# Performance work log

Measured on AMD Instinct MI355X. Metric: run time of the kernel, lower is better.

## Reference

```python
import jax, jax.numpy as jnp
import numpy as np

K = 32
TEMPERATURE = 0.1
RTOL, ATOL = 1e-5, 1e-5


def _embed(x, W1, b1, W2, b2, W3, b3):
    h = jax.nn.gelu(x @ W1.T + b1, approximate=False)
    h = jax.nn.gelu(h @ W2.T + b2, approximate=False)
    return jax.nn.sigmoid(h @ W3.T + b3)


def setup_inputs() -> dict:
    key = jax.random.key(0)
    ks = jax.random.split(key, 9)
    Q, N, D_IN, D_E = 256, 16384, 256, 64
    s = lambda fan_in: 1.0 / np.sqrt(fan_in)
    return {
        "x": jax.random.normal(ks[0], (Q, D_IN), jnp.float32),
        "support_x": jax.random.normal(ks[1], (N, D_IN), jnp.float32),
        "support_labels": jax.random.uniform(ks[2], (N, 1), jnp.float32),
        "W1": jax.random.normal(ks[3], (D_E, D_IN), jnp.float32) * s(D_IN),
        "b1": jax.random.normal(ks[4], (D_E,), jnp.float32) * s(D_IN),
        "W2": jax.random.normal(ks[5], (D_E, D_E), jnp.float32) * s(D_E),
        "b2": jax.random.normal(ks[6], (D_E,), jnp.float32) * s(D_E),
        "W3": jax.random.normal(ks[7], (D_E, D_E), jnp.float32) * s(D_E),
        "b3": jax.random.normal(ks[8], (D_E,), jnp.float32) * s(D_E),
    }


def reference(x, support_x, support_labels, W1, b1, W2, b2, W3, b3):
    # query embeddings [Q, D]; support embeddings [N, D] (set_support is no_grad)
    q = _embed(x, W1, b1, W2, b2, W3, b3)
    s = jax.lax.stop_gradient(_embed(support_x, W1, b1, W2, b2, W3, b3))
    # torch.cdist p=2 via expanded squared distances
    d2 = (jnp.sum(q * q, -1)[:, None] + jnp.sum(s * s, -1)[None, :]
          - 2.0 * (q @ s.T))
    dist = jnp.sqrt(jnp.maximum(d2, 0.0))  # [Q, N]
    # isclose mask: |q - s| <= atol + rtol*|s|, all over feature dim
    close = jnp.abs(q[:, None, :] - s[None, :, :]) <= (ATOL + RTOL * jnp.abs(s)[None, :, :])
    mask = jnp.all(close, axis=-1)  # [Q, N]
    dist = jnp.where(mask, jnp.inf, dist)
    # top-k smallest distances
    neg_top, idx = jax.lax.top_k(-dist, K)  # [Q, K]
    topd = -neg_top
    neighbor_labels = support_labels[idx].squeeze(-1)  # [Q, K]
    weights = jax.nn.softmax(-topd / TEMPERATURE, axis=1)
    return jnp.sum(weights * neighbor_labels, axis=1)  # [Q]
```

## Files before the change

### kernel.cpp

```cpp
#include <hip/hip_runtime.h>
#include <math.h>

#define D_IN   256
#define D_E    64
#define N_SUP  16384
#define NQ     256
#define KSEL   32
#define RTOLC  1e-5f
#define ATOLC  1e-5f
#define INV_T  10.0f

#define CHUNK  512
#define NCH    32
#define QG     16
#define NQG    16

typedef unsigned long long ull;

__device__ __forceinline__ float gelu_exact(float x) {
    return 0.5f * x * (1.0f + erff(x * 0.70710678118654752440f));
}

__global__ __launch_bounds__(128) void embed_kernel(
    const float* __restrict__ sx, const float* __restrict__ x,
    const float* __restrict__ W1, const float* __restrict__ b1,
    const float* __restrict__ W2, const float* __restrict__ b2,
    const float* __restrict__ W3, const float* __restrict__ b3,
    float* __restrict__ s_emb, float* __restrict__ s_norm,
    float* __restrict__ q_emb, float* __restrict__ q_norm)
{
    __shared__ float xc[2][64][36];
    __shared__ float wc[2][64][68];
    __shared__ float nsq[32][17];

    const int tid = threadIdx.x;
    const int rg  = tid >> 4;
    const int fg  = tid & 15;
    const bool isq = blockIdx.x >= (N_SUP / 32);
    const int rowbase = isq ? (int)(blockIdx.x - N_SUP / 32) * 32
                            : (int)blockIdx.x * 32;
    const float* src = (isq ? x : sx) + (size_t)rowbase * D_IN;

    #define STAGE_X(kc_, b_)                                                   \
        {                                                                      \
            _Pragma("unroll")                                                  \
            for (int i_ = 0; i_ < 4; ++i_) {                                   \
                int g_ = i_ * 128 + tid;                                       \
                int row_ = g_ >> 4, c4_ = g_ & 15;                             \
                float4 v_ = *reinterpret_cast<const float4*>(                  \
                    src + (size_t)row_ * D_IN + (kc_) * 64 + c4_ * 4);         \
                xc[b_][c4_ * 4 + 0][row_] = v_.x;                              \
                xc[b_][c4_ * 4 + 1][row_] = v_.y;                              \
                xc[b_][c4_ * 4 + 2][row_] = v_.z;                              \
                xc[b_][c4_ * 4 + 3][row_] = v_.w;                              \
            }                                                                  \
        }
    #define STAGE_W1(kc_, b_)                                                  \
        {                                                                      \
            _Pragma("unroll")                                                  \
            for (int i_ = 0; i_ < 8; ++i_) {                                   \
                int g_ = i_ * 128 + tid;                                       \
                int f_ = g_ >> 4, c4_ = g_ & 15;                               \
                float4 w_ = *reinterpret_cast<const float4*>(                  \
                    W1 + (size_t)f_ * D_IN + (kc_) * 64 + c4_ * 4);            \
                wc[b_][c4_ * 4 + 0][f_] = w_.x;                                \
                wc[b_][c4_ * 4 + 1][f_] = w_.y;                                \
                wc[b_][c4_ * 4 + 2][f_] = w_.z;                                \
                wc[b_][c4_ * 4 + 3][f_] = w_.w;                                \
            }                                                                  \
        }
    #define STAGE_WSQ(Wp_, b_)                                                 \
        {                                                                      \
            _Pragma("unroll")                                                  \
            for (int i_ = 0; i_ < 8; ++i_) {                                   \
                int g_ = i_ * 128 + tid;                                       \
                int f_ = g_ >> 4, c4_ = g_ & 15;                               \
                float4 w_ = *reinterpret_cast<const float4*>(                  \
                    (Wp_) + (size_t)f_ * D_E + c4_ * 4);                       \
                wc[b_][c4_ * 4 + 0][f_] = w_.x;                                \
                wc[b_][c4_ * 4 + 1][f_] = w_.y;                                \
                wc[b_][c4_ * 4 + 2][f_] = w_.z;                                \
                wc[b_][c4_ * 4 + 3][f_] = w_.w;                                \
            }                                                                  \
        }
    #define GEMM64(XB_, WB_, ACC_)                                             \
        {                                                                      \
            _Pragma("unroll 8")                                                \
            for (int k_ = 0; k_ < 64; ++k_) {                                  \
                float4 xv_ = *reinterpret_cast<const float4*>(&XB_[k_][rg * 4]); \
                float4 wv_ = *reinterpret_cast<const float4*>(&WB_[k_][fg * 4]); \
                ACC_[0][0] = fmaf(wv_.x, xv_.x, ACC_[0][0]);                   \
                ACC_[0][1] = fmaf(wv_.y, xv_.x, ACC_[0][1]);                   \
                ACC_[0][2] = fmaf(wv_.z, xv_.x, ACC_[0][2]);                   \
                ACC_[0][3] = fmaf(wv_.w, xv_.x, ACC_[0][3]);                   \
                ACC_[1][0] = fmaf(wv_.x, xv_.y, ACC_[1][0]);                   \
                ACC_[1][1] = fmaf(wv_.y, xv_.y, ACC_[1][1]);                   \
                ACC_[1][2] = fmaf(wv_.z, xv_.y, ACC_[1][2]);                   \
                ACC_[1][3] = fmaf(wv_.w, xv_.y, ACC_[1][3]);                   \
                ACC_[2][0] = fmaf(wv_.x, xv_.z, ACC_[2][0]);                   \
                ACC_[2][1] = fmaf(wv_.y, xv_.z, ACC_[2][1]);                   \
                ACC_[2][2] = fmaf(wv_.z, xv_.z, ACC_[2][2]);                   \
                ACC_[2][3] = fmaf(wv_.w, xv_.z, ACC_[2][3]);                   \
                ACC_[3][0] = fmaf(wv_.x, xv_.w, ACC_[3][0]);                   \
                ACC_[3][1] = fmaf(wv_.y, xv_.w, ACC_[3][1]);                   \
                ACC_[3][2] = fmaf(wv_.z, xv_.w, ACC_[3][2]);                   \
                ACC_[3][3] = fmaf(wv_.w, xv_.w, ACC_[3][3]);                   \
            }                                                                  \
        }

    float4 bv1 = *reinterpret_cast<const float4*>(b1 + fg * 4);
    float acc[4][4];
    #pragma unroll
    for (int j = 0; j < 4; ++j) {
        acc[j][0] = bv1.x; acc[j][1] = bv1.y; acc[j][2] = bv1.z; acc[j][3] = bv1.w;
    }
    STAGE_X(0, 0); STAGE_W1(0, 0);
    __syncthreads();
    #pragma unroll
    for (int kc = 0; kc < 4; ++kc) {
        const int b = kc & 1;
        if (kc < 3) { STAGE_X(kc + 1, b ^ 1); STAGE_W1(kc + 1, b ^ 1); }
        GEMM64(xc[b], wc[b], acc);
        __syncthreads();
    }

    #pragma unroll
    for (int j = 0; j < 4; ++j)
        #pragma unroll
        for (int i = 0; i < 4; ++i)
            xc[0][fg * 4 + i][rg * 4 + j] = gelu_exact(acc[j][i]);
    STAGE_WSQ(W2, 0);
    STAGE_WSQ(W3, 1);
    __syncthreads();

    float4 bv2 = *reinterpret_cast<const float4*>(b2 + fg * 4);
    float a2[4][4];
    #pragma unroll
    for (int j = 0; j < 4; ++j) {
        a2[j][0] = bv2.x; a2[j][1] = bv2.y; a2[j][2] = bv2.z; a2[j][3] = bv2.w;
    }
    GEMM64(xc[0], wc[0], a2);
    #pragma unroll
    for (int j = 0; j < 4; ++j)
        #pragma unroll
        for (int i = 0; i < 4; ++i)
            xc[1][fg * 4 + i][rg * 4 + j] = gelu_exact(a2[j][i]);
    __syncthreads();

    float4 bv3 = *reinterpret_cast<const float4*>(b3 + fg * 4);
    float a3[4][4];
    #pragma unroll
    for (int j = 0; j < 4; ++j) {
        a3[j][0] = bv3.x; a3[j][1] = bv3.y; a3[j][2] = bv3.z; a3[j][3] = bv3.w;
    }
    GEMM64(xc[1], wc[1], a3);

    float* E   = isq ? q_emb  : s_emb;
    float* Nrm = isq ? q_norm : s_norm;
    #pragma unroll
    for (int j = 0; j < 4; ++j) {
        float e0 = 1.0f / (1.0f + expf(-a3[j][0]));
        float e1 = 1.0f / (1.0f + expf(-a3[j][1]));
        float e2 = 1.0f / (1.0f + expf(-a3[j][2]));
        float e3 = 1.0f / (1.0f + expf(-a3[j][3]));
        *reinterpret_cast<float4*>(E + (size_t)(rowbase + rg * 4 + j) * D_E + fg * 4)
            = make_float4(e0, e1, e2, e3);
        a3[j][0] = fmaf(e0, e0, fmaf(e1, e1, fmaf(e2, e2, e3 * e3)));
    }
    #pragma unroll
    for (int j = 0; j < 4; ++j) nsq[rg * 4 + j][fg] = a3[j][0];
    __syncthreads();
    if (tid < 32) {
        float s = 0.0f;
        #pragma unroll
        for (int g = 0; g < 16; ++g) s += nsq[tid][g];
        Nrm[rowbase + tid] = s;
    }
    #undef STAGE_X
    #undef STAGE_W1
    #undef STAGE_WSQ
    #undef GEMM64
}

__global__ __launch_bounds__(512, 1) void knn_phaseA(
    const float* __restrict__ s_emb, const float* __restrict__ s_norm,
    const float* __restrict__ q_emb, const float* __restrict__ q_norm,
    const float* __restrict__ labels, ull* __restrict__ cand)
{
    __shared__ float tile[2][64 * 68];
    __shared__ ull   win_l[QG][KSEL];

    const int tid  = threadIdx.x;
    const int lane = tid & 63;
    const int wid  = tid >> 6;
    const int qg   = blockIdx.x >> 5;
    const int sc   = blockIdx.x & 31;
    const int qiu  = __builtin_amdgcn_readfirstlane(qg * QG + 2 * wid);
    const float* q0 = q_emb + (size_t)qiu * D_E;
    const float* q1 = q0 + D_E;
    const float  qn0 = q_norm[qiu];
    const float  qn1 = q_norm[qiu + 1];

    #pragma unroll
    for (int i = 0; i < 2; ++i) {
        int g = i * 512 + tid;
        int row = g >> 4, c4 = g & 15;
        float4 v = *reinterpret_cast<const float4*>(
            s_emb + (size_t)(sc * CHUNK + row) * D_E + c4 * 4);
        *reinterpret_cast<float4*>(&tile[0][row * 68 + c4 * 4]) = v;
    }
    __syncthreads();

    float d2a[8], d2b[8];
    #pragma unroll
    for (int s = 0; s < 8; ++s) {
        const int b = s & 1;
        float4 p0, p1;
        if (s < 7) {
            p0 = *reinterpret_cast<const float4*>(
                s_emb + (size_t)(sc * CHUNK + (s + 1) * 64 + (tid >> 4)) * D_E + (tid & 15) * 4);
            p1 = *reinterpret_cast<const float4*>(
                s_emb + (size_t)(sc * CHUNK + (s + 1) * 64 + ((512 + tid) >> 4)) * D_E + (tid & 15) * 4);
        }
        const float* tr = &tile[b][lane * 68];
        float a0 = 0.0f, a1 = 0.0f;
        #pragma unroll
        for (int c = 0; c < 16; ++c) {
            float4 sv = *reinterpret_cast<const float4*>(tr + c * 4);
            a0 = fmaf(q0[c * 4 + 0], sv.x, a0);
            a0 = fmaf(q0[c * 4 + 1], sv.y, a0);
            a0 = fmaf(q0[c * 4 + 2], sv.z, a0);
            a0 = fmaf(q0[c * 4 + 3], sv.w, a0);
            a1 = fmaf(q1[c * 4 + 0], sv.x, a1);
            a1 = fmaf(q1[c * 4 + 1], sv.y, a1);
            a1 = fmaf(q1[c * 4 + 2], sv.z, a1);
            a1 = fmaf(q1[c * 4 + 3], sv.w, a1);
        }
        const int grow = sc * CHUNK + s * 64 + lane;
        const float sn = s_norm[grow];
        float d20 = fmaxf(qn0 + sn - 2.0f * a0, 0.0f);
        float d21 = fmaxf(qn1 + sn - 2.0f * a1, 0.0f);
        if (d20 < 1e-3f) {
            bool close = true;
            for (int k = 0; k < D_E; ++k) {
                float svk = tr[k];
                close = close && (fabsf(q0[k] - svk) <= (ATOLC + RTOLC * fabsf(svk)));
            }
            if (close) d20 = INFINITY;
        }
        if (d21 < 1e-3f) {
            bool close = true;
            for (int k = 0; k < D_E; ++k) {
                float svk = tr[k];
                close = close && (fabsf(q1[k] - svk) <= (ATOLC + RTOLC * fabsf(svk)));
            }
            if (close) d21 = INFINITY;
        }
        d2a[s] = d20;
        d2b[s] = d21;
        if (s < 7) {
            *reinterpret_cast<float4*>(&tile[b ^ 1][(tid >> 4) * 68 + (tid & 15) * 4]) = p0;
            *reinterpret_cast<float4*>(&tile[b ^ 1][((512 + tid) >> 4) * 68 + (tid & 15) * 4]) = p1;
        }
        __syncthreads();
    }

    const int h  = lane >> 5;
    const unsigned l5 = lane & 31;
    ull sk[16];
    #pragma unroll
    for (int j = 0; j < 8; ++j) {
        float ta  = __shfl_xor(d2a[j], 32);
        float tbx = __shfl_xor(d2b[j], 32);
        float vlo = h ? tbx : d2a[j];
        float vhi = h ? d2b[j] : ta;
        unsigned rlo = (unsigned)(j * 64) + l5;
        sk[j]     = ((ull)__float_as_uint(vlo) << 9) | rlo;
        sk[j + 8] = ((ull)__float_as_uint(vhi) << 9) | (rlo + 32);
    }

    #pragma unroll
    for (int k = 2; k <= 16; k <<= 1) {
        #pragma unroll
        for (int j = k >> 1; j > 0; j >>= 1) {
            #pragma unroll
            for (int i = 0; i < 16; ++i) {
                int ixj = i ^ j;
                if (ixj > i) {
                    ull a_ = sk[i], b_ = sk[ixj];
                    bool up = (i & k) == 0;
                    bool c_ = up ? (b_ < a_) : (a_ < b_);
                    sk[i] = c_ ? b_ : a_; sk[ixj] = c_ ? a_ : b_;
                }
            }
        }
    }

    ull lkey = sk[0];
    for (int it = 0; it < KSEL; ++it) {
        unsigned lv = (unsigned)(lkey >> 9);
        unsigned m = lv;
        #pragma unroll
        for (int off = 1; off < 32; off <<= 1) {
            unsigned o = __shfl_xor(m, off);
            m = o < m ? o : m;
        }
        ull tb = __ballot(lv == m);
        bool cond;
        if (__popcll(tb) != 2) {
            unsigned rr = (lv == m) ? (unsigned)(lkey & 511u) : 0xffffffffu;
            unsigned rm = rr;
            #pragma unroll
            for (int off = 1; off < 32; off <<= 1) {
                unsigned o = __shfl_xor(rm, off);
                rm = o < rm ? o : rm;
            }
            cond = (lv == m) && ((unsigned)(lkey & 511u) == rm);
        } else {
            cond = (lv == m);
        }
        if (cond) {
            win_l[2 * wid + h][it] = lkey;
            #pragma unroll
            for (int j = 0; j < 15; ++j) sk[j] = sk[j + 1];
            sk[15] = ~0ull;
            lkey = sk[0];
        }
    }

    {
        const int e = (int)l5;
        ull m = win_l[2 * wid + h][e];
        unsigned gidx = (unsigned)(sc * CHUNK) + (unsigned)(m & 511u);
        float lab = labels[gidx];
        ull* dst = cand + ((size_t)(qg * QG + 2 * wid + h) * NCH + sc) * KSEL;
        dst[e] = ((ull)(unsigned)(m >> 9) << 32) | (ull)__float_as_uint(lab);
    }
}

__global__ __launch_bounds__(256) void knn_phaseB(
    const ull* __restrict__ cand, float* __restrict__ out)
{
    const int lane = threadIdx.x & 63;
    const int wid  = threadIdx.x >> 6;
    const int q    = blockIdx.x * 4 + wid;

    const bool act = lane < NCH;
    const ull* lst = cand + ((size_t)q * NCH + (lane & 31)) * KSEL;
    int ptr = 0;
    ull cur = act ? lst[0] : ~0ull;

    float d0 = 0.0f, sw = 0.0f, sl = 0.0f;
    for (int it = 0; it < KSEL; ++it) {
        unsigned mv = (unsigned)(cur >> 32);
        unsigned ml = (unsigned)cur;
        #pragma unroll
        for (int off = 1; off < 32; off <<= 1) {
            unsigned ov = __shfl_xor(mv, off);
            unsigned ol = __shfl_xor(ml, off);
            bool take = (ov < mv) || (ov == mv && (lane & off));
            mv = take ? ov : mv;
            ml = take ? ol : ml;
        }
        ull bl = __ballot(act && (unsigned)(cur >> 32) == mv);
        int wl = (int)(__ffsll((long long)bl) - 1);
        if (lane == wl) {
            ++ptr;
            cur = (ptr < KSEL) ? lst[ptr] : ~0ull;
        }
        if (lane == 0) {
            float d = sqrtf(__uint_as_float(mv));
            if (it == 0) d0 = d;
            float w = expf((d0 - d) * INV_T);
            sw += w;
            sl += w * __uint_as_float(ml);
        }
    }
    if (lane == 0) out[q] = sl / sw;
}

extern "C" void kernel_launch(void* const* d_in, const int* in_sizes, int n_in,
                              void* d_out, int out_size, void* d_ws, size_t ws_size,
                              hipStream_t stream) {
    const float* x      = (const float*)d_in[0];
    const float* sx     = (const float*)d_in[1];
    const float* labels = (const float*)d_in[2];
    const float* W1     = (const float*)d_in[3];
    const float* b1     = (const float*)d_in[4];
    const float* W2     = (const float*)d_in[5];
    const float* b2     = (const float*)d_in[6];
    const float* W3     = (const float*)d_in[7];
    const float* b3     = (const float*)d_in[8];
    float* out = (float*)d_out;

    float* ws     = (float*)d_ws;
    float* s_emb  = ws;
    float* s_norm = s_emb + (size_t)N_SUP * D_E;
    float* q_emb  = s_norm + N_SUP;
    float* q_norm = q_emb + (size_t)NQ * D_E;
    ull*   cand   = (ull*)(q_norm + NQ);

    embed_kernel<<<(N_SUP + NQ) / 32, 128, 0, stream>>>(
        sx, x, W1, b1, W2, b2, W3, b3, s_emb, s_norm, q_emb, q_norm);
    knn_phaseA<<<NQG * NCH, 512, 0, stream>>>(s_emb, s_norm, q_emb, q_norm,
                                              labels, cand);
    knn_phaseB<<<NQ / 4, 256, 0, stream>>>(cand, out);
}
```

Measured before the change: 102.9 us.

## Pre-transpose MLP weights and compute embeddings with direct global weight reads

Adds a small kernel that transposes W1, W2 and W3 into feature-contiguous layouts in the workspace on every call. The embedding kernel drops its LDS double-buffered tiling and its 4x4 register blocking. It now runs 256 threads per block, each computing 2 rows by 4 features, with weights read straight from global memory or cache. The intent is to remove the cost of staging and transposing tiles in shared memory. In exchange it pays an extra launch, lower register reuse and more global or L1 load traffic per FMA, and it relies on wavefront lockstep for the shared hidden-activation buffer, which has no block barriers between layers.

Result: slower. 109.7 us (+6.6%).

```diff
diff --git a/kernel.cpp b/kernel.cpp
--- a/kernel.cpp
+++ b/kernel.cpp
@@ -21,165 +21,135 @@
     return 0.5f * x * (1.0f + erff(x * 0.70710678118654752440f));
 }
 
-__global__ __launch_bounds__(128) void embed_kernel(
+__global__ __launch_bounds__(256) void prep_w(
+    const float* __restrict__ W1, const float* __restrict__ W2,
+    const float* __restrict__ W3,
+    float* __restrict__ W1T, float* __restrict__ W2T, float* __restrict__ W3T)
+{
+    const int t = blockIdx.x * 256 + threadIdx.x;
+    const int stride = gridDim.x * 256;
+    for (int o = t; o < D_E * D_IN; o += stride) {
+        int f = o >> 8, k = o & 255;
+        W1T[k * D_E + f] = W1[o];
+    }
+    for (int o = t; o < D_E * D_E; o += stride) {
+        int f = o >> 6, k = o & 63;
+        W2T[k * D_E + f] = W2[o];
+        W3T[k * D_E + f] = W3[o];
+    }
+}
+
+__global__ __launch_bounds__(256) void embed_kernel(
     const float* __restrict__ sx, const float* __restrict__ x,
-    const float* __restrict__ W1, const float* __restrict__ b1,
-    const float* __restrict__ W2, const float* __restrict__ b2,
-    const float* __restrict__ W3, const float* __restrict__ b3,
+    const float* __restrict__ W1T, const float* __restrict__ b1,
+    const float* __restrict__ W2T, const float* __restrict__ b2,
+    const float* __restrict__ W3T, const float* __restrict__ b3,
     float* __restrict__ s_emb, float* __restrict__ s_norm,
     float* __restrict__ q_emb, float* __restrict__ q_norm)
 {
-    __shared__ float xc[2][64][36];
-    __shared__ float wc[2][64][68];
+    __shared__ float hx[32][68];
     __shared__ float nsq[32][17];
 
     const int tid = threadIdx.x;
-    const int rg  = tid >> 4;
+    const int rp  = tid >> 4;
     const int fg  = tid & 15;
     const bool isq = blockIdx.x >= (N_SUP / 32);
-    const int rowbase = isq ? (int)(blockIdx.x - N_SUP / 32) * 32
-                            : (int)blockIdx.x * 32;
-    const float* src = (isq ? x : sx) + (size_t)rowbase * D_IN;
-
-    #define STAGE_X(kc_, b_)                                                   \
-        {                                                                      \
-            _Pragma("unroll")                                                  \
-            for (int i_ = 0; i_ < 4; ++i_) {                                   \
-                int g_ = i_ * 128 + tid;                                       \
-                int row_ = g_ >> 4, c4_ = g_ & 15;                             \
-                float4 v_ = *reinterpret_cast<const float4*>(                  \
-                    src + (size_t)row_ * D_IN + (kc_) * 64 + c4_ * 4);         \
-                xc[b_][c4_ * 4 + 0][row_] = v_.x;                              \
-                xc[b_][c4_ * 4 + 1][row_] = v_.y;                              \
-                xc[b_][c4_ * 4 + 2][row_] = v_.z;                              \
-                xc[b_][c4_ * 4 + 3][row_] = v_.w;                              \
-            }                                                                  \
-        }
-    #define STAGE_W1(kc_, b_)                                                  \
-        {                                                                      \
-            _Pragma("unroll")                                                  \
-            for (int i_ = 0; i_ < 8; ++i_) {                                   \
-                int g_ = i_ * 128 + tid;                                       \
-                int f_ = g_ >> 4, c4_ = g_ & 15;                               \
-                float4 w_ = *reinterpret_cast<const float4*>(                  \
-                    W1 + (size_t)f_ * D_IN + (kc_) * 64 + c4_ * 4);            \
-                wc[b_][c4_ * 4 + 0][f_] = w_.x;                                \
-                wc[b_][c4_ * 4 + 1][f_] = w_.y;                                \
-                wc[b_][c4_ * 4 + 2][f_] = w_.z;                                \
-                wc[b_][c4_ * 4 + 3][f_] = w_.w;                                \
-            }                                                                  \
-        }
-    #define STAGE_WSQ(Wp_, b_)                                                 \
-        {                                                                      \
-            _Pragma("unroll")                                                  \
-            for (int i_ = 0; i_ < 8; ++i_) {                                   \
-                int g_ = i_ * 128 + tid;                                       \
-                int f_ = g_ >> 4, c4_ = g_ & 15;                               \
-                float4 w_ = *reinterpret_cast<const float4*>(                  \
-                    (Wp_) + (size_t)f_ * D_E + c4_ * 4);                       \
-                wc[b_][c4_ * 4 + 0][f_] = w_.x;                                \
-                wc[b_][c4_ * 4 + 1][f_] = w_.y;                                \
-                wc[b_][c4_ * 4 + 2][f_] = w_.z;                                \
-                wc[b_][c4_ * 4 + 3][f_] = w_.w;                                \
-            }                                                                  \
-        }
-    #define GEMM64(XB_, WB_, ACC_)                                             \
-        {                                                                      \
-            _Pragma("unroll 8")                                                \
-            for (int k_ = 0; k_ < 64; ++k_) {                                  \
-                float4 xv_ = *reinterpret_cast<const float4*>(&XB_[k_][rg * 4]); \
-                float4 wv_ = *reinterpret_cast<const float4*>(&WB_[k_][fg * 4]); \
-                ACC_[0][0] = fmaf(wv_.x, xv_.x, ACC_[0][0]);                   \
-                ACC_[0][1] = fmaf(wv_.y, xv_.x, ACC_[0][1]);                   \
-                ACC_[0][2] = fmaf(wv_.z, xv_.x, ACC_[0][2]);                   \
-                ACC_[0][3] = fmaf(wv_.w, xv_.x, ACC_[0][3]);                   \
-                ACC_[1][0] = fmaf(wv_.x, xv_.y, ACC_[1][0]);                   \
-                ACC_[1][1] = fmaf(wv_.y, xv_.y, ACC_[1][1]);                   \
-                ACC_[1][2] = fmaf(wv_.z, xv_.y, ACC_[1][2]);                   \
-                ACC_[1][3] = fmaf(wv_.w, xv_.y, ACC_[1][3]);                   \
-                ACC_[2][0] = fmaf(wv_.x, xv_.z, ACC_[2][0]);                   \
-                ACC_[2][1] = fmaf(wv_.y, xv_.z, ACC_[2][1]);                   \
-                ACC_[2][2] = fmaf(wv_.z, xv_.z, ACC_[2][2]);                   \
-                ACC_[2][3] = fmaf(wv_.w, xv_.z, ACC_[2][3]);                   \
-                ACC_[3][0] = fmaf(wv_.x, xv_.w, ACC_[3][0]);                   \
-                ACC_[3][1] = fmaf(wv_.y, xv_.w, ACC_[3][1]);                   \
-                ACC_[3][2] = fmaf(wv_.z, xv_.w, ACC_[3][2]);                   \
-                ACC_[3][3] = fmaf(wv_.w, xv_.w, ACC_[3][3]);                   \
-            }                                                                  \
-        }
-
-    float4 bv1 = *reinterpret_cast<const float4*>(b1 + fg * 4);
-    float acc[4][4];
-    #pragma unroll
-    for (int j = 0; j < 4; ++j) {
-        acc[j][0] = bv1.x; acc[j][1] = bv1.y; acc[j][2] = bv1.z; acc[j][3] = bv1.w;
-    }
-    STAGE_X(0, 0); STAGE_W1(0, 0);
-    __syncthreads();
-    #pragma unroll
-    for (int kc = 0; kc < 4; ++kc) {
-        const int b = kc & 1;
-        if (kc < 3) { STAGE_X(kc + 1, b ^ 1); STAGE_W1(kc + 1, b ^ 1); }
-        GEMM64(xc[b], wc[b], acc);
-        __syncthreads();
-    }
-
-    #pragma unroll
-    for (int j = 0; j < 4; ++j)
-        #pragma unroll
-        for (int i = 0; i < 4; ++i)
-            xc[0][fg * 4 + i][rg * 4 + j] = gelu_exact(acc[j][i]);
-    STAGE_WSQ(W2, 0);
-    STAGE_WSQ(W3, 1);
-    __syncthreads();
-
-    float4 bv2 = *reinterpret_cast<const float4*>(b2 + fg * 4);
-    float a2[4][4];
-    #pragma unroll
-    for (int j = 0; j < 4; ++j) {
-        a2[j][0] = bv2.x; a2[j][1] = bv2.y; a2[j][2] = bv2.z; a2[j][3] = bv2.w;
-    }
-    GEMM64(xc[0], wc[0], a2);
-    #pragma unroll
-    for (int j = 0; j < 4; ++j)
-        #pragma unroll
-        for (int i = 0; i < 4; ++i)
-            xc[1][fg * 4 + i][rg * 4 + j] = gelu_exact(a2[j][i]);
-    __syncthreads();
-
-    float4 bv3 = *reinterpret_cast<const float4*>(b3 + fg * 4);
-    float a3[4][4];
-    #pragma unroll
-    for (int j = 0; j < 4; ++j) {
-        a3[j][0] = bv3.x; a3[j][1] = bv3.y; a3[j][2] = bv3.z; a3[j][3] = bv3.w;
-    }
-    GEMM64(xc[1], wc[1], a3);
+    const int rowb = (isq ? (int)blockIdx.x - N_SUP / 32 : (int)blockIdx.x) * 32;
+    const float* src = (isq ? x : sx) + (size_t)rowb * D_IN;
+    const float4* X4  = reinterpret_cast<const float4*>(src);
+    const float4* W14 = reinterpret_cast<const float4*>(W1T);
+    const float4* W24 = reinterpret_cast<const float4*>(W2T);
+    const float4* W34 = reinterpret_cast<const float4*>(W3T);
+    const int r0 = 2 * rp, r1 = 2 * rp + 1;
+
+    #define FMA4(acc_, w_, xs_)                                                \
+        acc_.x = fmaf(w_.x, xs_, acc_.x); acc_.y = fmaf(w_.y, xs_, acc_.y);    \
+        acc_.z = fmaf(w_.z, xs_, acc_.z); acc_.w = fmaf(w_.w, xs_, acc_.w);
+
+    float4 acc0 = reinterpret_cast<const float4*>(b1)[fg];
+    float4 acc1 = acc0;
+    #pragma unroll 4
+    for (int k4 = 0; k4 < 64; ++k4) {
+        float4 xa = X4[r0 * 64 + k4];
+        float4 xb = X4[r1 * 64 + k4];
+        float4 wa = W14[(4 * k4 + 0) * 16 + fg];
+        float4 wb = W14[(4 * k4 + 1) * 16 + fg];
+        float4 wc = W14[(4 * k4 + 2) * 16 + fg];
+        float4 wd = W14[(4 * k4 + 3) * 16 + fg];
+        FMA4(acc0, wa, xa.x); FMA4(acc0, wb, xa.y);
+        FMA4(acc0, wc, xa.z); FMA4(acc0, wd, xa.w);
+        FMA4(acc1, wa, xb.x); FMA4(acc1, wb, xb.y);
+        FMA4(acc1, wc, xb.z); FMA4(acc1, wd, xb.w);
+    }
+    *reinterpret_cast<float4*>(&hx[r0][fg * 4]) = make_float4(
+        gelu_exact(acc0.x), gelu_exact(acc0.y), gelu_exact(acc0.z), gelu_exact(acc0.w));
+    *reinterpret_cast<float4*>(&hx[r1][fg * 4]) = make_float4(
+        gelu_exact(acc1.x), gelu_exact(acc1.y), gelu_exact(acc1.z), gelu_exact(acc1.w));
+
+    float4 c0 = reinterpret_cast<const float4*>(b2)[fg];
+    float4 c1 = c0;
+    #pragma unroll 4
+    for (int k4 = 0; k4 < 16; ++k4) {
+        float4 xa = *reinterpret_cast<const float4*>(&hx[r0][k4 * 4]);
+        float4 xb = *reinterpret_cast<const float4*>(&hx[r1][k4 * 4]);
+        float4 wa = W24[(4 * k4 + 0) * 16 + fg];
+        float4 wb = W24[(4 * k4 + 1) * 16 + fg];
+        float4 wc = W24[(4 * k4 + 2) * 16 + fg];
+        float4 wd = W24[(4 * k4 + 3) * 16 + fg];
+        FMA4(c0, wa, xa.x); FMA4(c0, wb, xa.y);
+        FMA4(c0, wc, xa.z); FMA4(c0, wd, xa.w);
+        FMA4(c1, wa, xb.x); FMA4(c1, wb, xb.y);
+        FMA4(c1, wc, xb.z); FMA4(c1, wd, xb.w);
+    }
+    *reinterpret_cast<float4*>(&hx[r0][fg * 4]) = make_float4(
+        gelu_exact(c0.x), gelu_exact(c0.y), gelu_exact(c0.z), gelu_exact(c0.w));
+    *reinterpret_cast<float4*>(&hx[r1][fg * 4]) = make_float4(
+        gelu_exact(c1.x), gelu_exact(c1.y), gelu_exact(c1.z), gelu_exact(c1.w));
+
+    float4 d0 = reinterpret_cast<const float4*>(b3)[fg];
+    float4 d1 = d0;
+    #pragma unroll 4
+    for (int k4 = 0; k4 < 16; ++k4) {
+        float4 xa = *reinterpret_cast<const float4*>(&hx[r0][k4 * 4]);
+        float4 xb = *reinterpret_cast<const float4*>(&hx[r1][k4 * 4]);
+        float4 wa = W34[(4 * k4 + 0) * 16 + fg];
+        float4 wb = W34[(4 * k4 + 1) * 16 + fg];
+        float4 wc = W34[(4 * k4 + 2) * 16 + fg];
+        float4 wd = W34[(4 * k4 + 3) * 16 + fg];
+        FMA4(d0, wa, xa.x); FMA4(d0, wb, xa.y);
+        FMA4(d0, wc, xa.z); FMA4(d0, wd, xa.w);
+        FMA4(d1, wa, xb.x); FMA4(d1, wb, xb.y);
+        FMA4(d1, wc, xb.z); FMA4(d1, wd, xb.w);
+    }
+    #undef FMA4
 
     float* E   = isq ? q_emb  : s_emb;
     float* Nrm = isq ? q_norm : s_norm;
-    #pragma unroll
-    for (int j = 0; j < 4; ++j) {
-        float e0 = 1.0f / (1.0f + expf(-a3[j][0]));
-        float e1 = 1.0f / (1.0f + expf(-a3[j][1]));
-        float e2 = 1.0f / (1.0f + expf(-a3[j][2]));
-        float e3 = 1.0f / (1.0f + expf(-a3[j][3]));
-        *reinterpret_cast<float4*>(E + (size_t)(rowbase + rg * 4 + j) * D_E + fg * 4)
-            = make_float4(e0, e1, e2, e3);
-        a3[j][0] = fmaf(e0, e0, fmaf(e1, e1, fmaf(e2, e2, e3 * e3)));
-    }
-    #pragma unroll
-    for (int j = 0; j < 4; ++j) nsq[rg * 4 + j][fg] = a3[j][0];
+    {
+        float e0 = 1.0f / (1.0f + expf(-d0.x));
+        float e1 = 1.0f / (1.0f + expf(-d0.y));
+        float e2 = 1.0f / (1.0f + expf(-d0.z));
+        float e3 = 1.0f / (1.0f + expf(-d0.w));
+        *reinterpret_cast<float4*>(E + (size_t)(rowb + r0) * D_E + fg * 4) =
+            make_float4(e0, e1, e2, e3);
+        nsq[r0][fg] = fmaf(e0, e0, fmaf(e1, e1, fmaf(e2, e2, e3 * e3)));
+    }
+    {
+        float e0 = 1.0f / (1.0f + expf(-d1.x));
+        float e1 = 1.0f / (1.0f + expf(-d1.y));
+        float e2 = 1.0f / (1.0f + expf(-d1.z));
+        float e3 = 1.0f / (1.0f + expf(-d1.w));
+        *reinterpret_cast<float4*>(E + (size_t)(rowb + r1) * D_E + fg * 4) =
+            make_float4(e0, e1, e2, e3);
+        nsq[r1][fg] = fmaf(e0, e0, fmaf(e1, e1, fmaf(e2, e2, e3 * e3)));
+    }
     __syncthreads();
     if (tid < 32) {
         float s = 0.0f;
         #pragma unroll
         for (int g = 0; g < 16; ++g) s += nsq[tid][g];
-        Nrm[rowbase + tid] = s;
-    }
-    #undef STAGE_X
-    #undef STAGE_W1
-    #undef STAGE_WSQ
-    #undef GEMM64
+        Nrm[rowb + tid] = s;
+    }
 }
 
 __global__ __launch_bounds__(512, 1) void knn_phaseA(
@@ -399,9 +369,13 @@
     float* q_emb  = s_norm + N_SUP;
     float* q_norm = q_emb + (size_t)NQ * D_E;
     ull*   cand   = (ull*)(q_norm + NQ);
-
-    embed_kernel<<<(N_SUP + NQ) / 32, 128, 0, stream>>>(
-        sx, x, W1, b1, W2, b2, W3, b3, s_emb, s_norm, q_emb, q_norm);
+    float* W1T    = (float*)(cand + (size_t)NQ * NCH * KSEL);
+    float* W2T    = W1T + D_IN * D_E;
+    float* W3T    = W2T + D_E * D_E;
+
+    prep_w<<<32, 256, 0, stream>>>(W1, W2, W3, W1T, W2T, W3T);
+    embed_kernel<<<(N_SUP + NQ) / 32, 256, 0, stream>>>(
+        sx, x, W1T, b1, W2T, b2, W3T, b3, s_emb, s_norm, q_emb, q_norm);
     knn_phaseA<<<NQG * NCH, 512, 0, stream>>>(s_emb, s_norm, q_emb, q_norm,
                                               labels, cand);
     knn_phaseB<<<NQ / 4, 256, 0, stream>>>(cand, out);
```
